# Performance work log

Hardware: AMD Instinct MI355X
Metric: run time of the kernel (lower is better)

## Reference

```python
import jax, jax.numpy as jnp
import numpy as np

SCALE = 128.0            # input_size
CONF_THRESH = 0.75
IOU_THRESH = 0.3
MAX_DET = 100
SCORE_CLIP = 100.0
N_ANCHORS = 4194304


def setup_inputs() -> dict:
    key = jax.random.key(0)
    k1, k2, k3 = jax.random.split(key, 3)
    raw_boxes = jax.random.normal(k1, (1, N_ANCHORS, 4), dtype=jnp.float32)
    raw_scores = jax.random.normal(k2, (1, N_ANCHORS, 1), dtype=jnp.float32)
    # anchors: [x_center, y_center, w, h] in [0, 1]
    anchors = jax.random.uniform(k3, (N_ANCHORS, 4), dtype=jnp.float32)
    return {"raw_boxes": raw_boxes, "raw_scores": raw_scores, "anchors": anchors}


def _iou_matrix(boxes):
    # boxes: (K, 4) as [ymin, xmin, ymax, xmax]
    ymin, xmin, ymax, xmax = boxes[:, 0], boxes[:, 1], boxes[:, 2], boxes[:, 3]
    area = (ymax - ymin) * (xmax - xmin)
    iy = jnp.clip(jnp.minimum(ymax[:, None], ymax[None, :]) - jnp.maximum(ymin[:, None], ymin[None, :]), 0.0)
    ix = jnp.clip(jnp.minimum(xmax[:, None], xmax[None, :]) - jnp.maximum(xmin[:, None], xmin[None, :]), 0.0)
    inter = iy * ix
    union = area[:, None] + area[None, :] - inter
    return inter / jnp.maximum(union, 1e-9)


def reference(raw_boxes, raw_scores, anchors):
    # --- box decode (anchors: [xc, yc, w, h]) ---
    x_center = raw_boxes[..., 0] / SCALE * anchors[:, 2] + anchors[:, 0]
    y_center = raw_boxes[..., 1] / SCALE * anchors[:, 3] + anchors[:, 1]
    w = raw_boxes[..., 2] / SCALE * anchors[:, 2]
    h = raw_boxes[..., 3] / SCALE * anchors[:, 3]
    half_h, half_w = h * 0.5, w * 0.5
    y_min, x_min = y_center - half_h, x_center - half_w
    y_max, x_max = y_center + half_h, x_center + half_w
    # sanitize: min/max per coordinate pair (matches torch.minimum/maximum restack)
    boxes = jnp.stack([
        jnp.minimum(y_min, y_max), jnp.minimum(x_min, x_max),
        jnp.maximum(y_min, y_max), jnp.maximum(x_min, x_max)], axis=-1)  # (B, N, 4)

    scores = jnp.clip(raw_scores, -SCORE_CLIP, SCORE_CLIP)
    scores = jax.nn.sigmoid(scores)[..., 0]  # (B, N)

    boxes0, scores0 = boxes[0], scores[0]
    topk_scores, topk_idx = jax.lax.top_k(scores0, MAX_DET)  # sorted desc
    topk_boxes = boxes0[topk_idx]  # (K, 4) ymin,xmin,ymax,xmax

    # --- greedy NMS on the sorted top-K ---
    iou = _iou_matrix(topk_boxes)
    idx = jnp.arange(MAX_DET)

    def body(keep, i):
        active = keep[i]
        suppress = active & (iou[i] > IOU_THRESH) & (idx > i)
        return keep & ~suppress, None

    keep, _ = jax.lax.scan(body, jnp.ones((MAX_DET,), dtype=bool), idx)

    valid = keep & (topk_scores >= CONF_THRESH)
    # compact valid detections to the front (stable), zero-pad the rest
    order = jnp.argsort(jnp.logical_not(valid).astype(jnp.int32), stable=True)
    dets = jnp.concatenate([topk_boxes, topk_scores[:, None]], axis=-1)[order]
    dets = jnp.where(valid[order][:, None], dets, 0.0)
    return dets  # (MAX_DET, 5): [ymin, xmin, ymax, xmax, score], padded rows are zero
```

## Files before the change

kernel.cpp:

```cpp
#include <hip/hip_runtime.h>
#include <stdint.h>

#define N_ANCH 4194304
#define KDET 100
#define CAND_MAX 1024
#define NBLK 1024
#define BCAP 16
#define THRESH_F 3.9f
#define KEYS_OFF  4096
#define BOXES_OFF 16384

__device__ __forceinline__ uint32_t fkey(float f) {
    uint32_t u = __float_as_uint(f);
    return (u & 0x80000000u) ? ~u : (u | 0x80000000u);
}

__device__ __forceinline__ float4 decode_box(const float4* rb4, const float4* an4,
                                             uint32_t idx) {
    float4 rb = rb4[idx];
    float4 an = an4[idx];
    float xc = rb.x * (1.0f / 128.0f) * an.z + an.x;
    float yc = rb.y * (1.0f / 128.0f) * an.w + an.y;
    float w  = rb.z * (1.0f / 128.0f) * an.z;
    float h  = rb.w * (1.0f / 128.0f) * an.w;
    float y0 = yc - 0.5f * h, y1 = yc + 0.5f * h;
    float x0 = xc - 0.5f * w, x1 = xc + 0.5f * w;
    float4 r;
    r.x = fminf(y0, y1);
    r.y = fminf(x0, x1);
    r.z = fmaxf(y0, y1);
    r.w = fmaxf(x0, x1);
    return r;
}

__global__ void __launch_bounds__(256) k_collect(
    const float* __restrict__ scores, const float* __restrict__ raw_boxes,
    const float* __restrict__ anchors, uint32_t* __restrict__ gcnt,
    uint64_t* __restrict__ ckeys, float4* __restrict__ cboxes)
{
    __shared__ uint32_t lcnt, lbase;
    __shared__ uint64_t lkey[BCAP];
    __shared__ float4 lbox[BCAP];
    int t = threadIdx.x;
    if (t == 0) lcnt = 0;
    __syncthreads();
    const uint32_t keymin = fkey(THRESH_F);
    int tid = blockIdx.x * 256 + t;
    const float4* s4 = (const float4*)scores;
    const float4* rb4 = (const float4*)raw_boxes;
    const float4* an4 = (const float4*)anchors;
    #pragma unroll
    for (int k = 0; k < 4; ++k) {
        int i = tid + k * (NBLK * 256);
        float4 v = s4[i];
        uint32_t k0 = fkey(v.x), k1 = fkey(v.y), k2 = fkey(v.z), k3 = fkey(v.w);
        uint32_t kmax = max(max(k0, k1), max(k2, k3));
        if (kmax >= keymin) {
            uint32_t base = (uint32_t)i * 4u;
            if (k0 >= keymin) { uint32_t p = atomicAdd(&lcnt, 1u); if (p < BCAP) { lkey[p] = ((uint64_t)k0 << 32) | (uint32_t)~(base + 0u); lbox[p] = decode_box(rb4, an4, base + 0u); } }
            if (k1 >= keymin) { uint32_t p = atomicAdd(&lcnt, 1u); if (p < BCAP) { lkey[p] = ((uint64_t)k1 << 32) | (uint32_t)~(base + 1u); lbox[p] = decode_box(rb4, an4, base + 1u); } }
            if (k2 >= keymin) { uint32_t p = atomicAdd(&lcnt, 1u); if (p < BCAP) { lkey[p] = ((uint64_t)k2 << 32) | (uint32_t)~(base + 2u); lbox[p] = decode_box(rb4, an4, base + 2u); } }
            if (k3 >= keymin) { uint32_t p = atomicAdd(&lcnt, 1u); if (p < BCAP) { lkey[p] = ((uint64_t)k3 << 32) | (uint32_t)~(base + 3u); lbox[p] = decode_box(rb4, an4, base + 3u); } }
        }
    }
    __syncthreads();
    uint32_t c = min(lcnt, (uint32_t)BCAP);
    if (t == 0 && c > 0) lbase = atomicAdd(gcnt, c);
    __syncthreads();
    if (t < (int)c) {
        uint32_t p = lbase + t;
        if (p < CAND_MAX) { ckeys[p] = lkey[t]; cboxes[p] = lbox[t]; }
    }
}

__global__ void __launch_bounds__(256) k_final(
    const uint32_t* __restrict__ gcnt, const uint64_t* __restrict__ ckeys,
    const float4* __restrict__ cboxes, float* __restrict__ out)
{
    __shared__ uint64_t cands_s[CAND_MAX];
    __shared__ float4 cbox_s[CAND_MAX];
    __shared__ uint64_t top_s[KDET];
    __shared__ uint16_t top_src[KDET];
    __shared__ float by0[KDET], bx0[KDET], by1[KDET], bx1[KDET], sc_s[KDET];
    __shared__ uint64_t adj0[KDET], adj1[KDET];
    __shared__ uint64_t vm0_s, vm1_s;
    __shared__ int M_s;
    int t = threadIdx.x;

    if (t == 0) {
        uint32_t m = *gcnt;
        M_s = (m > CAND_MAX) ? CAND_MAX : (int)m;
    }
    if (t < KDET) top_s[t] = 0ULL;
    __syncthreads();
    int M = M_s;

    for (int j = t; j < M; j += 256) {
        cands_s[j] = ckeys[j];
        cbox_s[j] = cboxes[j];
    }
    __syncthreads();

    for (int j = t; j < M; j += 256) {
        uint64_t my = cands_s[j];
        int r = 0, k = 0;
        for (; k + 4 <= M; k += 4) {
            r += (cands_s[k + 0] > my);
            r += (cands_s[k + 1] > my);
            r += (cands_s[k + 2] > my);
            r += (cands_s[k + 3] > my);
        }
        for (; k < M; ++k) r += (cands_s[k] > my);
        if (r < KDET) { top_s[r] = my; top_src[r] = (uint16_t)j; }
    }
    __syncthreads();

    float ty0 = 0.f, tx0 = 0.f, ty1 = 0.f, tx1 = 0.f;
    if (t < KDET) {
        uint64_t my = top_s[t];
        if (my != 0ULL) {
            float rs = __uint_as_float((uint32_t)(my >> 32) & 0x7FFFFFFFu);
            rs = fminf(rs, 100.0f);
            sc_s[t] = 1.0f / (1.0f + __expf(-rs));
            float4 b = cbox_s[top_src[t]];
            ty0 = b.x; tx0 = b.y; ty1 = b.z; tx1 = b.w;
        } else {
            sc_s[t] = -1.0f;
        }
        by0[t] = ty0; bx0[t] = tx0; by1[t] = ty1; bx1[t] = tx1;
    }
    __syncthreads();

    uint64_t a0 = 0ULL, a1 = 0ULL;
    if (t < KDET) {
        float myarea = (ty1 - ty0) * (tx1 - tx0);
        for (int j = 0; j < KDET; ++j) {
            float jy0 = by0[j], jx0 = bx0[j], jy1 = by1[j], jx1 = bx1[j];
            float aj = (jy1 - jy0) * (jx1 - jx0);
            float iy = fmaxf(fminf(ty1, jy1) - fmaxf(ty0, jy0), 0.0f);
            float ix = fmaxf(fminf(tx1, jx1) - fmaxf(tx0, jx0), 0.0f);
            float inter = iy * ix;
            float iou = inter / fmaxf(myarea + aj - inter, 1e-9f);
            if (iou > 0.3f) { if (j < 64) a0 |= (1ULL << j); else a1 |= (1ULL << (j - 64)); }
        }
        adj0[t] = a0; adj1[t] = a1;
    }
    __syncthreads();

    if (t < 64) {
        uint64_t r1a0 = 0ULL, r1a1 = 0ULL;
        if (t < KDET - 64) { r1a0 = adj0[t + 64]; r1a1 = adj1[t + 64]; }
        uint64_t keep0 = ~0ULL, keep1 = (1ULL << (KDET - 64)) - 1ULL;
        for (int i = 0; i < KDET; ++i) {
            uint64_t b0, b1;
            if (i < 64) { b0 = __shfl(a0, i);        b1 = __shfl(a1, i); }
            else        { b0 = __shfl(r1a0, i - 64); b1 = __shfl(r1a1, i - 64); }
            bool alive = (i < 64) ? ((keep0 >> i) & 1ULL) : ((keep1 >> (i - 64)) & 1ULL);
            if (alive) {
                if (i < 64) {
                    b0 &= (i < 63) ? (~0ULL << (i + 1)) : 0ULL;
                } else {
                    b0 = 0ULL;
                    b1 &= (~0ULL << (i - 63));
                }
                keep0 &= ~b0; keep1 &= ~b1;
            }
        }
        bool v_lo = ((keep0 >> t) & 1ULL) && (sc_s[t] >= 0.75f);
        uint64_t vm0 = __ballot(v_lo);
        bool v_hi = (t < KDET - 64) && ((keep1 >> t) & 1ULL) && (sc_s[t + 64] >= 0.75f);
        uint64_t vm1 = __ballot(v_hi);
        if (t == 0) { vm0_s = vm0; vm1_s = vm1; }
    }
    __syncthreads();

    for (int i = t; i < KDET * 5; i += 256) out[i] = 0.0f;
    __syncthreads();

    if (t < KDET) {
        uint64_t vm0 = vm0_s, vm1 = vm1_s;
        bool valid = (t < 64) ? ((vm0 >> t) & 1ULL) : ((vm1 >> (t - 64)) & 1ULL);
        if (valid) {
            int r = (t < 64)
                ? __popcll(vm0 & ((t == 0) ? 0ULL : (~0ULL >> (64 - t))))
                : __popcll(vm0) + __popcll(vm1 & ((t == 64) ? 0ULL : (~0ULL >> (128 - t))));
            out[r * 5 + 0] = by0[t];
            out[r * 5 + 1] = bx0[t];
            out[r * 5 + 2] = by1[t];
            out[r * 5 + 3] = bx1[t];
            out[r * 5 + 4] = sc_s[t];
        }
    }
}

extern "C" void kernel_launch(void* const* d_in, const int* in_sizes, int n_in,
                              void* d_out, int out_size, void* d_ws, size_t ws_size,
                              hipStream_t stream) {
    const float* raw_boxes  = (const float*)d_in[0];
    const float* raw_scores = (const float*)d_in[1];
    const float* anchors    = (const float*)d_in[2];
    float* out = (float*)d_out;
    uint32_t* gcnt = (uint32_t*)d_ws;
    uint64_t* ckeys = (uint64_t*)((char*)d_ws + KEYS_OFF);
    float4* cboxes = (float4*)((char*)d_ws + BOXES_OFF);

    hipMemsetAsync(gcnt, 0, sizeof(uint32_t), stream);
    k_collect<<<NBLK, 256, 0, stream>>>(raw_scores, raw_boxes, anchors,
                                        gcnt, ckeys, cboxes);
    k_final<<<1, 256, 0, stream>>>(gcnt, ckeys, cboxes, out);
}
```

Measured before the change: 166.1 us.

## Fuse collect and final NMS kernels via last-block ticket

Merges the candidate-collection and top-K/NMS kernels into one launch. The block that takes the last ticket from a global atomic counter runs the final selection stage. Candidate stores and loads go through device-scope atomics so they are visible across blocks without a second launch. The aim is to remove one kernel launch and its gap, at the cost of atomic traffic and extra shared memory held by every block. It also unrolls the rank loop wider and packs the boxes as float4.

New measurement: 174.9 us. +5.3%, slower.

```diff
diff --git a/kernel.cpp b/kernel.cpp
--- a/kernel.cpp
+++ b/kernel.cpp
@@ -8,7 +8,7 @@
 #define BCAP 16
 #define THRESH_F 3.9f
 #define KEYS_OFF  4096
-#define BOXES_OFF 16384
+#define BOX_OFF   16384
 
 __device__ __forceinline__ uint32_t fkey(float f) {
     uint32_t u = __float_as_uint(f);
@@ -33,62 +33,74 @@
     return r;
 }
 
-__global__ void __launch_bounds__(256) k_collect(
+__global__ void __launch_bounds__(256) k_fused(
     const float* __restrict__ scores, const float* __restrict__ raw_boxes,
     const float* __restrict__ anchors, uint32_t* __restrict__ gcnt,
-    uint64_t* __restrict__ ckeys, float4* __restrict__ cboxes)
+    unsigned long long* __restrict__ ckeys, unsigned long long* __restrict__ cbox,
+    float* __restrict__ out)
 {
-    __shared__ uint32_t lcnt, lbase;
+    __shared__ uint32_t lcnt, lbase, ticket_s;
     __shared__ uint64_t lkey[BCAP];
     __shared__ float4 lbox[BCAP];
+
     int t = threadIdx.x;
     if (t == 0) lcnt = 0;
     __syncthreads();
-    const uint32_t keymin = fkey(THRESH_F);
-    int tid = blockIdx.x * 256 + t;
-    const float4* s4 = (const float4*)scores;
-    const float4* rb4 = (const float4*)raw_boxes;
-    const float4* an4 = (const float4*)anchors;
-    #pragma unroll
-    for (int k = 0; k < 4; ++k) {
-        int i = tid + k * (NBLK * 256);
-        float4 v = s4[i];
-        uint32_t k0 = fkey(v.x), k1 = fkey(v.y), k2 = fkey(v.z), k3 = fkey(v.w);
-        uint32_t kmax = max(max(k0, k1), max(k2, k3));
-        if (kmax >= keymin) {
-            uint32_t base = (uint32_t)i * 4u;
-            if (k0 >= keymin) { uint32_t p = atomicAdd(&lcnt, 1u); if (p < BCAP) { lkey[p] = ((uint64_t)k0 << 32) | (uint32_t)~(base + 0u); lbox[p] = decode_box(rb4, an4, base + 0u); } }
-            if (k1 >= keymin) { uint32_t p = atomicAdd(&lcnt, 1u); if (p < BCAP) { lkey[p] = ((uint64_t)k1 << 32) | (uint32_t)~(base + 1u); lbox[p] = decode_box(rb4, an4, base + 1u); } }
-            if (k2 >= keymin) { uint32_t p = atomicAdd(&lcnt, 1u); if (p < BCAP) { lkey[p] = ((uint64_t)k2 << 32) | (uint32_t)~(base + 2u); lbox[p] = decode_box(rb4, an4, base + 2u); } }
-            if (k3 >= keymin) { uint32_t p = atomicAdd(&lcnt, 1u); if (p < BCAP) { lkey[p] = ((uint64_t)k3 << 32) | (uint32_t)~(base + 3u); lbox[p] = decode_box(rb4, an4, base + 3u); } }
+
+    {
+        const uint32_t keymin = fkey(THRESH_F);
+        int tid = blockIdx.x * 256 + t;
+        const float4* s4 = (const float4*)scores;
+        const float4* rb4 = (const float4*)raw_boxes;
+        const float4* an4 = (const float4*)anchors;
+        #pragma unroll
+        for (int k = 0; k < 4; ++k) {
+            int i = tid + k * (NBLK * 256);
+            float4 v = s4[i];
+            uint32_t k0 = fkey(v.x), k1 = fkey(v.y), k2 = fkey(v.z), k3 = fkey(v.w);
+            uint32_t kmax = max(max(k0, k1), max(k2, k3));
+            if (kmax >= keymin) {
+                uint32_t base = (uint32_t)i * 4u;
+                if (k0 >= keymin) { uint32_t p = atomicAdd(&lcnt, 1u); if (p < BCAP) { lkey[p] = ((uint64_t)k0 << 32) | (uint32_t)~(base + 0u); lbox[p] = decode_box(rb4, an4, base + 0u); } }
+                if (k1 >= keymin) { uint32_t p = atomicAdd(&lcnt, 1u); if (p < BCAP) { lkey[p] = ((uint64_t)k1 << 32) | (uint32_t)~(base + 1u); lbox[p] = decode_box(rb4, an4, base + 1u); } }
+                if (k2 >= keymin) { uint32_t p = atomicAdd(&lcnt, 1u); if (p < BCAP) { lkey[p] = ((uint64_t)k2 << 32) | (uint32_t)~(base + 2u); lbox[p] = decode_box(rb4, an4, base + 2u); } }
+                if (k3 >= keymin) { uint32_t p = atomicAdd(&lcnt, 1u); if (p < BCAP) { lkey[p] = ((uint64_t)k3 << 32) | (uint32_t)~(base + 3u); lbox[p] = decode_box(rb4, an4, base + 3u); } }
+            }
         }
     }
     __syncthreads();
     uint32_t c = min(lcnt, (uint32_t)BCAP);
-    if (t == 0 && c > 0) lbase = atomicAdd(gcnt, c);
+    if (t == 0) lbase = (c > 0) ? atomicAdd(&gcnt[0], c) : 0u;
     __syncthreads();
     if (t < (int)c) {
         uint32_t p = lbase + t;
-        if (p < CAND_MAX) { ckeys[p] = lkey[t]; cboxes[p] = lbox[t]; }
-    }
-}
-
-__global__ void __launch_bounds__(256) k_final(
-    const uint32_t* __restrict__ gcnt, const uint64_t* __restrict__ ckeys,
-    const float4* __restrict__ cboxes, float* __restrict__ out)
-{
+        if (p < CAND_MAX) {
+            atomicExch(&ckeys[p], (unsigned long long)lkey[t]);
+            float4 b = lbox[t];
+            unsigned long long lo = ((unsigned long long)__float_as_uint(b.y) << 32) | __float_as_uint(b.x);
+            unsigned long long hi = ((unsigned long long)__float_as_uint(b.w) << 32) | __float_as_uint(b.z);
+            atomicExch(&cbox[2u * p + 0u], lo);
+            atomicExch(&cbox[2u * p + 1u], hi);
+        }
+    }
+    asm volatile("s_waitcnt vmcnt(0)" ::: "memory");
+    __syncthreads();
+    if (t == 0) ticket_s = atomicAdd(&gcnt[1], 1u);
+    __syncthreads();
+    if (ticket_s != (uint32_t)(NBLK - 1)) return;
+
     __shared__ uint64_t cands_s[CAND_MAX];
     __shared__ float4 cbox_s[CAND_MAX];
     __shared__ uint64_t top_s[KDET];
     __shared__ uint16_t top_src[KDET];
-    __shared__ float by0[KDET], bx0[KDET], by1[KDET], bx1[KDET], sc_s[KDET];
+    __shared__ float4 tb_s[KDET];
+    __shared__ float sc_s[KDET];
     __shared__ uint64_t adj0[KDET], adj1[KDET];
     __shared__ uint64_t vm0_s, vm1_s;
     __shared__ int M_s;
-    int t = threadIdx.x;
 
     if (t == 0) {
-        uint32_t m = *gcnt;
+        uint32_t m = atomicAdd(&gcnt[0], 0u);
         M_s = (m > CAND_MAX) ? CAND_MAX : (int)m;
     }
     if (t < KDET) top_s[t] = 0ULL;
@@ -96,49 +108,60 @@
     int M = M_s;
 
     for (int j = t; j < M; j += 256) {
-        cands_s[j] = ckeys[j];
-        cbox_s[j] = cboxes[j];
+        cands_s[j] = atomicAdd(&ckeys[j], 0ULL);
+        unsigned long long lo = atomicAdd(&cbox[2u * j + 0u], 0ULL);
+        unsigned long long hi = atomicAdd(&cbox[2u * j + 1u], 0ULL);
+        float4 b;
+        b.x = __uint_as_float((uint32_t)lo);
+        b.y = __uint_as_float((uint32_t)(lo >> 32));
+        b.z = __uint_as_float((uint32_t)hi);
+        b.w = __uint_as_float((uint32_t)(hi >> 32));
+        cbox_s[j] = b;
     }
     __syncthreads();
 
     for (int j = t; j < M; j += 256) {
         uint64_t my = cands_s[j];
         int r = 0, k = 0;
-        for (; k + 4 <= M; k += 4) {
+        for (; k + 8 <= M; k += 8) {
             r += (cands_s[k + 0] > my);
             r += (cands_s[k + 1] > my);
             r += (cands_s[k + 2] > my);
             r += (cands_s[k + 3] > my);
+            r += (cands_s[k + 4] > my);
+            r += (cands_s[k + 5] > my);
+            r += (cands_s[k + 6] > my);
+            r += (cands_s[k + 7] > my);
         }
         for (; k < M; ++k) r += (cands_s[k] > my);
         if (r < KDET) { top_s[r] = my; top_src[r] = (uint16_t)j; }
     }
     __syncthreads();
 
-    float ty0 = 0.f, tx0 = 0.f, ty1 = 0.f, tx1 = 0.f;
+    float4 tb = make_float4(0.f, 0.f, 0.f, 0.f);
     if (t < KDET) {
         uint64_t my = top_s[t];
         if (my != 0ULL) {
             float rs = __uint_as_float((uint32_t)(my >> 32) & 0x7FFFFFFFu);
             rs = fminf(rs, 100.0f);
             sc_s[t] = 1.0f / (1.0f + __expf(-rs));
-            float4 b = cbox_s[top_src[t]];
-            ty0 = b.x; tx0 = b.y; ty1 = b.z; tx1 = b.w;
+            tb = cbox_s[top_src[t]];
         } else {
             sc_s[t] = -1.0f;
         }
-        by0[t] = ty0; bx0[t] = tx0; by1[t] = ty1; bx1[t] = tx1;
+        tb_s[t] = tb;
     }
     __syncthreads();
 
     uint64_t a0 = 0ULL, a1 = 0ULL;
     if (t < KDET) {
-        float myarea = (ty1 - ty0) * (tx1 - tx0);
+        float myarea = (tb.z - tb.x) * (tb.w - tb.y);
+        #pragma unroll 4
         for (int j = 0; j < KDET; ++j) {
-            float jy0 = by0[j], jx0 = bx0[j], jy1 = by1[j], jx1 = bx1[j];
-            float aj = (jy1 - jy0) * (jx1 - jx0);
-            float iy = fmaxf(fminf(ty1, jy1) - fmaxf(ty0, jy0), 0.0f);
-            float ix = fmaxf(fminf(tx1, jx1) - fmaxf(tx0, jx0), 0.0f);
+            float4 jb = tb_s[j];
+            float aj = (jb.z - jb.x) * (jb.w - jb.y);
+            float iy = fmaxf(fminf(tb.z, jb.z) - fmaxf(tb.x, jb.x), 0.0f);
+            float ix = fmaxf(fminf(tb.w, jb.w) - fmaxf(tb.y, jb.y), 0.0f);
             float inter = iy * ix;
             float iou = inter / fmaxf(myarea + aj - inter, 1e-9f);
             if (iou > 0.3f) { if (j < 64) a0 |= (1ULL << j); else a1 |= (1ULL << (j - 64)); }
@@ -184,10 +207,11 @@
             int r = (t < 64)
                 ? __popcll(vm0 & ((t == 0) ? 0ULL : (~0ULL >> (64 - t))))
                 : __popcll(vm0) + __popcll(vm1 & ((t == 64) ? 0ULL : (~0ULL >> (128 - t))));
-            out[r * 5 + 0] = by0[t];
-            out[r * 5 + 1] = bx0[t];
-            out[r * 5 + 2] = by1[t];
-            out[r * 5 + 3] = bx1[t];
+            float4 b = tb_s[t];
+            out[r * 5 + 0] = b.x;
+            out[r * 5 + 1] = b.y;
+            out[r * 5 + 2] = b.z;
+            out[r * 5 + 3] = b.w;
             out[r * 5 + 4] = sc_s[t];
         }
     }
@@ -201,11 +225,10 @@
     const float* anchors    = (const float*)d_in[2];
     float* out = (float*)d_out;
     uint32_t* gcnt = (uint32_t*)d_ws;
-    uint64_t* ckeys = (uint64_t*)((char*)d_ws + KEYS_OFF);
-    float4* cboxes = (float4*)((char*)d_ws + BOXES_OFF);
-
-    hipMemsetAsync(gcnt, 0, sizeof(uint32_t), stream);
-    k_collect<<<NBLK, 256, 0, stream>>>(raw_scores, raw_boxes, anchors,
-                                        gcnt, ckeys, cboxes);
-    k_final<<<1, 256, 0, stream>>>(gcnt, ckeys, cboxes, out);
-}
+    unsigned long long* ckeys = (unsigned long long*)((char*)d_ws + KEYS_OFF);
+    unsigned long long* cbox  = (unsigned long long*)((char*)d_ws + BOX_OFF);
+
+    hipMemsetAsync(gcnt, 0, 2 * sizeof(uint32_t), stream);
+    k_fused<<<NBLK, 256, 0, stream>>>(raw_scores, raw_boxes, anchors,
+                                      gcnt, ckeys, cbox, out);
+}
```
